# Kernel optimization log

Hardware: AMD Instinct MI355X
Metric: run time of the kernel (lower is better)

Reference implementation:

```python
import jax, jax.numpy as jnp
import numpy as np

# BTT dims for in=out=4096, square mode: m=n=64, a=b=64, rank=8
M, N, A, B_BLK, RANK = 64, 64, 64, 64, 8
OUT_FEATURES = M * A  # 4096


def setup_inputs() -> dict:
    key = jax.random.key(0)
    k_x, k_r, k_l = jax.random.split(key, 3)
    x = jax.random.normal(k_x, (4, 1024, 4096), dtype=jnp.float32)
    # btt_r: (n, b, m*rank); btt_l: (m, rank*n, a)
    btt_r = jax.random.normal(k_r, (N, B_BLK, M * RANK), dtype=jnp.float32) * 0.02
    btt_l = jax.random.normal(k_l, (M, RANK * N, A), dtype=jnp.float32) * 0.02
    bias = jnp.zeros((OUT_FEATURES,), dtype=jnp.float32)
    return {"x": x, "btt_r": btt_r, "btt_l": btt_l, "bias": bias}


def reference(x, btt_r, btt_l, bias):
    n, b, mr = btt_r.shape
    m, rn, a = btt_l.shape
    rank = mr // m
    orig_shape = x.shape
    xr = x.reshape(-1, n, b)          # (B, n, b)
    Bn = xr.shape[0]
    # first contraction: bmm over n blocks -> (n, B, m*rank)
    inner = jnp.einsum('Bnb,nbj->nBj', xr, btt_r)
    # reshape/permute exactly as torch: (n,B,m,r) -> (m,B,n,r) -> (m,B,n*r)
    inner = inner.reshape(n, Bn, m, rank).transpose(2, 1, 0, 3).reshape(m, Bn, rank * n)
    # second contraction: bmm over m blocks -> (B, m, a)
    out = jnp.einsum('mBk,mka->Bma', inner, btt_l)
    out = out.reshape(*orig_shape[:-1], m * a)
    return out + bias
```

## Files before the change

kernel.cpp:

```cpp
#include <hip/hip_runtime.h>


typedef float f32x16 __attribute__((ext_vector_type(16)));
typedef short short8 __attribute__((ext_vector_type(8)));

static __device__ __forceinline__ unsigned short f2b(float f) {
    union { float f; unsigned u; } a; a.f = f;
    unsigned u = a.u;
    unsigned r = u + 0x7fffu + ((u >> 16) & 1u);
    return (unsigned short)(r >> 16);
}

static __device__ __forceinline__ void load_lds_16(const void* gptr, void* lptr) {
    __builtin_amdgcn_global_load_lds(
        (const __attribute__((address_space(1))) unsigned int*)gptr,
        (__attribute__((address_space(3))) unsigned int*)lptr, 16, 0, 0);
}

__global__ __launch_bounds__(256) void prep_all(
    const float* __restrict__ x,
    const float* __restrict__ btt_r,
    const float* __restrict__ btt_l,
    unsigned short* __restrict__ xbt,
    unsigned short* __restrict__ Wtt,
    int nx)
{
    const int tid = threadIdx.x;
    if ((int)blockIdx.x < nx) {
        unsigned i = blockIdx.x * 256 + tid;
        int row = ((i >> 12) << 3) | (i & 7);
        int g   = (i >> 3) & 511;
        float4 v0 = *(const float4*)(x + (size_t)row * 4096 + g * 8);
        float4 v1 = *(const float4*)(x + (size_t)row * 4096 + g * 8 + 4);
        unsigned short o[8];
        o[0] = f2b(v0.x); o[1] = f2b(v0.y); o[2] = f2b(v0.z); o[3] = f2b(v0.w);
        o[4] = f2b(v1.x); o[5] = f2b(v1.y); o[6] = f2b(v1.z); o[7] = f2b(v1.w);
        int ks = g >> 1, half = g & 1;
        int rt = row >> 8, rb = (row >> 5) & 7, l31 = row & 31;
        size_t dst = ((((size_t)rt * 256 + ks) * 8 + rb) * 64 + half * 32 + l31) * 8;
        *(uint4*)(xbt + dst) = *(const uint4*)o;
        return;
    }
    __shared__ float Rs[64][8];
    __shared__ float Ls[8][64];
    const int wb = blockIdx.x - nx;
    const int m = wb >> 6, n = wb & 63;

    if (tid < 128) {
        int b = tid >> 1, rh = (tid & 1) * 4;
        float4 v = *(const float4*)(btt_r + (size_t)n * 32768 + (size_t)b * 512 + m * 8 + rh);
        *(float4*)&Rs[b][rh] = v;
    } else {
        int t2 = (tid - 128) * 4;
        float4 v = *(const float4*)(btt_l + (size_t)m * 32768 + n * 512 + t2);
        *(float4*)&(&Ls[0][0])[t2] = v;
    }
    __syncthreads();

    const int a  = tid >> 2;
    const int bg = (tid & 3) * 16;
    float la[8];
    #pragma unroll
    for (int r = 0; r < 8; ++r) la[r] = Ls[r][a];

    unsigned short o[16];
    #pragma unroll
    for (int bb = 0; bb < 16; ++bb) {
        float acc = 0.f;
        #pragma unroll
        for (int r = 0; r < 8; ++r) acc += Rs[bg + bb][r] * la[r];
        o[bb] = f2b(acc);
    }
    int col = m * 64 + a;
    int ct = col >> 8, rb = (col >> 5) & 7, l31 = col & 31;
    int ks = n * 4 + (bg >> 4);
    size_t dst = ((((size_t)ct * 256 + ks) * 8 + rb) * 64 + l31) * 8;
    *(uint4*)(Wtt + dst)           = *(const uint4*)&o[0];
    *(uint4*)(Wtt + dst + 32 * 8)  = *(const uint4*)&o[8];
}

__global__ __launch_bounds__(512, 2) void gemm_btt(
    const unsigned short* __restrict__ xbt,
    const unsigned short* __restrict__ Wtt,
    const float* __restrict__ bias,
    float* __restrict__ out)
{
    __shared__ unsigned short As[8][4096];
    __shared__ unsigned short Bs[8][4096];

    const int tid = threadIdx.x;
    const int bid = blockIdx.x;
    const int cpx = gridDim.x >> 3;
    const int swz = (bid & 7) * cpx + (bid >> 3);
    const int rt = swz >> 4;
    const int ct = swz & 15;

    const int wid = tid >> 6, l = tid & 63;
    const int l31 = l & 31, half = l >> 5;
    const int wr = wid >> 2;
    const int wc = wid & 3;

    const unsigned short* xa = xbt + (size_t)rt * (256 * 4096);
    const unsigned short* wa = Wtt + (size_t)ct * (256 * 4096);

    const int offA0 = ((wr * 4 + 0) * 64 + l) * 8;
    const int offA1 = ((wr * 4 + 1) * 64 + l) * 8;
    const int offA2 = ((wr * 4 + 2) * 64 + l) * 8;
    const int offA3 = ((wr * 4 + 3) * 64 + l) * 8;
    const int offB0 = ((wc * 2 + 0) * 64 + l) * 8;
    const int offB1 = ((wc * 2 + 1) * 64 + l) * 8;

    f32x16 acc[4][2];
    #pragma unroll
    for (int i = 0; i < 4; ++i)
        #pragma unroll
        for (int j = 0; j < 2; ++j)
            #pragma unroll
            for (int r = 0; r < 16; ++r)
                acc[i][j][r] = 0.f;

    #define STAGE(s) do {                                                    \
        load_lds_16(xa + (size_t)(s) * 4096 + tid * 8, &As[(s) & 7][tid * 8]); \
        load_lds_16(wa + (size_t)(s) * 4096 + tid * 8, &Bs[(s) & 7][tid * 8]); \
    } while (0)

    #define BARRIER() do {                                                   \
        asm volatile("s_waitcnt lgkmcnt(0)" ::: "memory");                   \
        __builtin_amdgcn_s_barrier();                                        \
        asm volatile("" ::: "memory");                                       \
    } while (0)

    #define SLICE(s) do {                                                    \
        const unsigned short* Ab = &As[(s) & 7][0];                          \
        const unsigned short* Bb = &Bs[(s) & 7][0];                          \
        short8 af0 = *(const short8*)(Ab + offA0);                           \
        short8 af1 = *(const short8*)(Ab + offA1);                           \
        short8 af2 = *(const short8*)(Ab + offA2);                           \
        short8 af3 = *(const short8*)(Ab + offA3);                           \
        short8 bf0 = *(const short8*)(Bb + offB0);                           \
        short8 bf1 = *(const short8*)(Bb + offB1);                           \
        __builtin_amdgcn_s_setprio(1);                                       \
        acc[0][0] = __builtin_amdgcn_mfma_f32_32x32x16_bf16(af0, bf0, acc[0][0], 0, 0, 0); \
        acc[0][1] = __builtin_amdgcn_mfma_f32_32x32x16_bf16(af0, bf1, acc[0][1], 0, 0, 0); \
        acc[1][0] = __builtin_amdgcn_mfma_f32_32x32x16_bf16(af1, bf0, acc[1][0], 0, 0, 0); \
        acc[1][1] = __builtin_amdgcn_mfma_f32_32x32x16_bf16(af1, bf1, acc[1][1], 0, 0, 0); \
        acc[2][0] = __builtin_amdgcn_mfma_f32_32x32x16_bf16(af2, bf0, acc[2][0], 0, 0, 0); \
        acc[2][1] = __builtin_amdgcn_mfma_f32_32x32x16_bf16(af2, bf1, acc[2][1], 0, 0, 0); \
        acc[3][0] = __builtin_amdgcn_mfma_f32_32x32x16_bf16(af3, bf0, acc[3][0], 0, 0, 0); \
        acc[3][1] = __builtin_amdgcn_mfma_f32_32x32x16_bf16(af3, bf1, acc[3][1], 0, 0, 0); \
        __builtin_amdgcn_s_setprio(0);                                       \
    } while (0)

    #pragma unroll
    for (int s = 0; s < 6; ++s) STAGE(s);
    asm volatile("s_waitcnt vmcnt(8)" ::: "memory");

    #pragma unroll 1
    for (int j = 0; j < 125; ++j) {
        const int s0 = 2 * j;
        BARRIER();
        STAGE(s0 + 6);
        STAGE(s0 + 7);
        asm volatile("s_waitcnt vmcnt(8)" ::: "memory");
        SLICE(s0);
        SLICE(s0 + 1);
    }
    BARRIER();
    asm volatile("s_waitcnt vmcnt(4)" ::: "memory");
    SLICE(250);
    SLICE(251);
    BARRIER();
    asm volatile("s_waitcnt vmcnt(0)" ::: "memory");
    SLICE(252);
    SLICE(253);
    BARRIER();
    SLICE(254);
    SLICE(255);

    const int rowTileBase = rt * 256 + wr * 128;
    const int colTileBase = ct * 256 + wc * 64;
    #pragma unroll
    for (int jn = 0; jn < 2; ++jn) {
        const int col = colTileBase + jn * 32 + l31;
        const float bv = bias[col];
        #pragma unroll
        for (int i = 0; i < 4; ++i) {
            const int rbase = rowTileBase + i * 32 + 4 * half;
            #pragma unroll
            for (int r = 0; r < 16; ++r) {
                int row = rbase + (r & 3) + 8 * (r >> 2);
                out[(size_t)row * 4096 + col] = acc[i][jn][r] + bv;
            }
        }
    }
    #undef STAGE
    #undef BARRIER
    #undef SLICE
}

extern "C" void kernel_launch(void* const* d_in, const int* in_sizes, int n_in,
                              void* d_out, int out_size, void* d_ws, size_t ws_size,
                              hipStream_t stream) {
    const float* x    = (const float*)d_in[0];
    const float* r    = (const float*)d_in[1];
    const float* l    = (const float*)d_in[2];
    const float* bias = (const float*)d_in[3];
    float* out = (float*)d_out;

    unsigned short* xbt = (unsigned short*)d_ws;
    unsigned short* Wtt = (unsigned short*)d_ws + (size_t)4096 * 4096;

    const int rows = in_sizes[0] / 4096;
    const int nx = rows * 4096 / 8 / 256;

    prep_all<<<dim3(nx + 4096), dim3(256), 0, stream>>>(x, r, l, xbt, Wtt, nx);
    gemm_btt<<<dim3((rows / 256) * 16), dim3(512), 0, stream>>>(xbt, Wtt, bias, out);
}
```

Before: 296.4 us.

## Restructure GEMM main loop into per-slice phases with 4-deep prefetch and XCD-local tile mapping

The main loop is rewritten so each slice issues its LDS fragment reads, then issues the next global-to-LDS prefetch, then waits and barriers before the MFMAs, with a second barrier after them. The prefetch depth drops from six slices to four, and the loop is unrolled eight-wide over fixed LDS slots. The block-to-tile mapping also changes so that each group of blocks sharing an XCD covers a 4x8 patch of row and column tiles, which should improve L2 reuse. The cost is two barriers per slice instead of one per two slices, plus a shallower prefetch, which could expose memory latency.

```diff
diff --git a/kernel.cpp b/kernel.cpp
--- a/kernel.cpp
+++ b/kernel.cpp
@@ -90,10 +90,9 @@
 
     const int tid = threadIdx.x;
     const int bid = blockIdx.x;
-    const int cpx = gridDim.x >> 3;
-    const int swz = (bid & 7) * cpx + (bid >> 3);
-    const int rt = swz >> 4;
-    const int ct = swz & 15;
+    const int jj = bid >> 3, xc = bid & 7;
+    const int rt = (xc >> 1) * 4 + (jj >> 3);
+    const int ct = (xc & 1) * 8 + (jj & 7);
 
     const int wid = tid >> 6, l = tid & 63;
     const int l31 = l & 31, half = l >> 5;
@@ -119,27 +118,25 @@
             for (int r = 0; r < 16; ++r)
                 acc[i][j][r] = 0.f;
 
-    #define STAGE(s) do {                                                    \
-        load_lds_16(xa + (size_t)(s) * 4096 + tid * 8, &As[(s) & 7][tid * 8]); \
-        load_lds_16(wa + (size_t)(s) * 4096 + tid * 8, &Bs[(s) & 7][tid * 8]); \
+    #define STAGE(s, slot) do {                                               \
+        load_lds_16(xa + (size_t)(s) * 4096 + tid * 8, &As[slot][tid * 8]);   \
+        load_lds_16(wa + (size_t)(s) * 4096 + tid * 8, &Bs[slot][tid * 8]);   \
     } while (0)
 
-    #define BARRIER() do {                                                   \
-        asm volatile("s_waitcnt lgkmcnt(0)" ::: "memory");                   \
-        __builtin_amdgcn_s_barrier();                                        \
-        asm volatile("" ::: "memory");                                       \
-    } while (0)
-
-    #define SLICE(s) do {                                                    \
-        const unsigned short* Ab = &As[(s) & 7][0];                          \
-        const unsigned short* Bb = &Bs[(s) & 7][0];                          \
-        short8 af0 = *(const short8*)(Ab + offA0);                           \
-        short8 af1 = *(const short8*)(Ab + offA1);                           \
-        short8 af2 = *(const short8*)(Ab + offA2);                           \
-        short8 af3 = *(const short8*)(Ab + offA3);                           \
-        short8 bf0 = *(const short8*)(Bb + offB0);                           \
-        short8 bf1 = *(const short8*)(Bb + offB1);                           \
-        __builtin_amdgcn_s_setprio(1);                                       \
+    #define PHASE(slot, STAGE_STMT, VMSTR) do {                               \
+        const unsigned short* Ab = &As[slot][0];                              \
+        const unsigned short* Bb = &Bs[slot][0];                              \
+        short8 af0 = *(const short8*)(Ab + offA0);                            \
+        short8 af1 = *(const short8*)(Ab + offA1);                            \
+        short8 af2 = *(const short8*)(Ab + offA2);                            \
+        short8 af3 = *(const short8*)(Ab + offA3);                            \
+        short8 bf0 = *(const short8*)(Bb + offB0);                            \
+        short8 bf1 = *(const short8*)(Bb + offB1);                            \
+        STAGE_STMT;                                                           \
+        asm volatile(VMSTR ::: "memory");                                     \
+        __builtin_amdgcn_s_barrier();                                         \
+        asm volatile("s_waitcnt lgkmcnt(0)" ::: "memory");                    \
+        __builtin_amdgcn_s_setprio(1);                                        \
         acc[0][0] = __builtin_amdgcn_mfma_f32_32x32x16_bf16(af0, bf0, acc[0][0], 0, 0, 0); \
         acc[0][1] = __builtin_amdgcn_mfma_f32_32x32x16_bf16(af0, bf1, acc[0][1], 0, 0, 0); \
         acc[1][0] = __builtin_amdgcn_mfma_f32_32x32x16_bf16(af1, bf0, acc[1][0], 0, 0, 0); \
@@ -148,34 +145,36 @@
         acc[2][1] = __builtin_amdgcn_mfma_f32_32x32x16_bf16(af2, bf1, acc[2][1], 0, 0, 0); \
         acc[3][0] = __builtin_amdgcn_mfma_f32_32x32x16_bf16(af3, bf0, acc[3][0], 0, 0, 0); \
         acc[3][1] = __builtin_amdgcn_mfma_f32_32x32x16_bf16(af3, bf1, acc[3][1], 0, 0, 0); \
-        __builtin_amdgcn_s_setprio(0);                                       \
+        __builtin_amdgcn_s_setprio(0);                                        \
+        __builtin_amdgcn_s_barrier();                                         \
+        asm volatile("" ::: "memory");                                        \
     } while (0)
 
-    #pragma unroll
-    for (int s = 0; s < 6; ++s) STAGE(s);
-    asm volatile("s_waitcnt vmcnt(8)" ::: "memory");
+    STAGE(0, 0); STAGE(1, 1); STAGE(2, 2); STAGE(3, 3);
+    asm volatile("s_waitcnt vmcnt(6)" ::: "memory");
+    __builtin_amdgcn_s_barrier();
+    asm volatile("" ::: "memory");
 
     #pragma unroll 1
-    for (int j = 0; j < 125; ++j) {
-        const int s0 = 2 * j;
-        BARRIER();
-        STAGE(s0 + 6);
-        STAGE(s0 + 7);
-        asm volatile("s_waitcnt vmcnt(8)" ::: "memory");
-        SLICE(s0);
-        SLICE(s0 + 1);
-    }
-    BARRIER();
-    asm volatile("s_waitcnt vmcnt(4)" ::: "memory");
-    SLICE(250);
-    SLICE(251);
-    BARRIER();
-    asm volatile("s_waitcnt vmcnt(0)" ::: "memory");
-    SLICE(252);
-    SLICE(253);
-    BARRIER();
-    SLICE(254);
-    SLICE(255);
+    for (int it = 0; it < 31; ++it) {
+        const int s0 = it * 8;
+        PHASE(0, STAGE(s0 + 4,  4), "s_waitcnt vmcnt(6)");
+        PHASE(1, STAGE(s0 + 5,  5), "s_waitcnt vmcnt(6)");
+        PHASE(2, STAGE(s0 + 6,  6), "s_waitcnt vmcnt(6)");
+        PHASE(3, STAGE(s0 + 7,  7), "s_waitcnt vmcnt(6)");
+        PHASE(4, STAGE(s0 + 8,  0), "s_waitcnt vmcnt(6)");
+        PHASE(5, STAGE(s0 + 9,  1), "s_waitcnt vmcnt(6)");
+        PHASE(6, STAGE(s0 + 10, 2), "s_waitcnt vmcnt(6)");
+        PHASE(7, STAGE(s0 + 11, 3), "s_waitcnt vmcnt(6)");
+    }
+    PHASE(0, STAGE(252, 4), "s_waitcnt vmcnt(6)");
+    PHASE(1, STAGE(253, 5), "s_waitcnt vmcnt(6)");
+    PHASE(2, STAGE(254, 6), "s_waitcnt vmcnt(6)");
+    PHASE(3, STAGE(255, 7), "s_waitcnt vmcnt(6)");
+    PHASE(4, ((void)0),     "s_waitcnt vmcnt(4)");
+    PHASE(5, ((void)0),     "s_waitcnt vmcnt(2)");
+    PHASE(6, ((void)0),     "s_waitcnt vmcnt(0)");
+    PHASE(7, ((void)0),     "s_waitcnt vmcnt(0)");
 
     const int rowTileBase = rt * 256 + wr * 128;
     const int colTileBase = ct * 256 + wc * 64;
@@ -194,8 +193,7 @@
         }
     }
     #undef STAGE
-    #undef BARRIER
-    #undef SLICE
+    #undef PHASE
 }
 
 extern "C" void kernel_launch(void* const* d_in, const int* in_sizes, int n_in,
```

After: 281.8 us. 1.05x faster.
